# Optimization experiments

Measured on AMD Instinct MI355X. Metric: run time of the kernel, lower is better.

## Reference

```python
import jax, jax.numpy as jnp
import numpy as np

NUM_HEADS = 8
WINDOW = 33  # must be odd for seq length to be preserved


def setup_inputs() -> dict:
    key = jax.random.key(0)
    ks = jax.random.split(key, 7)
    B, S, E = 4, 2048, 256
    sc = 1.0 / np.sqrt(E)
    return {
        "x": jax.random.normal(ks[0], (B, S, E), dtype=jnp.float32),
        "Wq": jax.random.normal(ks[1], (E, E), dtype=jnp.float32) * sc,
        "bq": jax.random.normal(ks[2], (E,), dtype=jnp.float32) * 0.01,
        "Wk": jax.random.normal(ks[3], (E, E), dtype=jnp.float32) * sc,
        "bk": jax.random.normal(ks[4], (E,), dtype=jnp.float32) * 0.01,
        "Wv": jax.random.normal(ks[5], (E, E), dtype=jnp.float32) * sc,
        "bv": jax.random.normal(ks[6], (E,), dtype=jnp.float32) * 0.01,
    }


def reference(x, Wq, bq, Wk, bk, Wv, bv):
    B, S, E = x.shape
    H = NUM_HEADS
    D = E // H
    W = WINDOW
    pad = (W - 1) // 2
    scale = D ** (-0.5)

    def heads(t):  # [B,S,E] -> [B,H,S,D]
        return t.reshape(B, S, H, D).transpose(0, 2, 1, 3)

    q = heads(x @ Wq + bq)
    k = heads(x @ Wk + bk)
    v = heads(x @ Wv + bv)

    K = S - W + 1  # number of k/v windows (unfold with step=1)
    kv_idx = jnp.arange(K)[:, None] + jnp.arange(W)[None, :]  # [K,W]
    k_unf = k[:, :, kv_idx, :]  # [B,H,K,W,D]
    v_unf = v[:, :, kv_idx, :]  # [B,H,K,W,D]

    q_pad = jnp.pad(q, ((0, 0), (0, 0), (pad, pad), (0, 0)))  # zero pad seq
    q_idx = jnp.arange(S)[:, None] + jnp.arange(W)[None, :]  # [S,W]
    q_unf = q_pad[:, :, q_idx, :]  # [B,H,S,W,D]

    # contract over BOTH window and head dim (faithful to the torch einsums)
    scores = jnp.einsum('bhqwd,bhkwd->bhqk', q_unf, k_unf) * scale  # [B,H,S,K]
    attn = jax.nn.softmax(scores, axis=-1)
    out = jnp.einsum('bhqk,bhkwd->bhqd', attn, v_unf)  # sums v over window too
    return out.transpose(0, 2, 1, 3).reshape(B, S, E)
```

## Files before the change

kernel.cpp:

```cpp
#include <hip/hip_runtime.h>
#include <hip/hip_bf16.h>
#include <math.h>

#define BB   4
#define SS   2048
#define EE   256
#define HH   8
#define DD   32
#define WW   33
#define KKN  (SS - WW + 1)
#define SCALE 0.17677669529663687f
#define FMAX 20.0f
#define SCALE2 0.25503486f
#define FM2    28.853900817779268f

typedef __attribute__((ext_vector_type(8))) short short8v;
typedef __attribute__((ext_vector_type(4))) short short4v;
typedef __attribute__((ext_vector_type(4))) float float4v;

__device__ __forceinline__ short f2bf(float f) {
    union { __hip_bfloat16 h; short s; } c;
    c.h = __float2bfloat16(f);
    return c.s;
}

__device__ __forceinline__ float bf2f(short h) {
    union { unsigned u; float f; } c;
    c.u = ((unsigned)(unsigned short)h) << 16;
    return c.f;
}

__device__ __forceinline__ short2 f2bf2(float a, float b) {
    union { __hip_bfloat162 h; short2 s; } c;
    float2 f; f.x = a; f.y = b;
    c.h = __float22bfloat162_rn(f);
    return c.s;
}

#if __has_builtin(__builtin_amdgcn_exp2f)
__device__ __forceinline__ float exp2_fast(float x) { return __builtin_amdgcn_exp2f(x); }
#else
__device__ __forceinline__ float exp2_fast(float x) { return __expf(x * 0.6931471805599453f); }
#endif

__global__ __launch_bounds__(256) void cvt_kernel(
    const float* __restrict__ x,
    const float* __restrict__ Wq, const float* __restrict__ Wk,
    short* __restrict__ xh, short* __restrict__ xl,
    short* __restrict__ wth, short* __restrict__ wtl)
{
    const int t  = threadIdx.x;
    const int bx = blockIdx.x;
    if (bx < 1024) {
        size_t i8 = ((size_t)bx * 256 + t) * 8;
        float4 f0 = *(const float4*)(x + i8);
        float4 f1 = *(const float4*)(x + i8 + 4);
        float f[8] = {f0.x, f0.y, f0.z, f0.w, f1.x, f1.y, f1.z, f1.w};
        short8v h, l;
#pragma unroll
        for (int j = 0; j < 8; j++) {
            short hb = f2bf(f[j]);
            h[j] = hb;
            l[j] = f2bf(f[j] - bf2f(hb));
        }
        *(short8v*)(xh + i8) = h;
        *(short8v*)(xl + i8) = l;
    } else {
        int o   = (bx - 1024) * 2048 + t * 8;
        int mat = o >> 16;
        int rem = o & 65535;
        int n = rem >> 8, k0 = rem & 255;
        const float* W = mat ? Wk : Wq;
        short8v h, l;
#pragma unroll
        for (int j = 0; j < 8; j++) {
            float f = W[(size_t)(k0 + j) * 256 + n];
            short hb = f2bf(f);
            h[j] = hb;
            l[j] = f2bf(f - bf2f(hb));
        }
        *(short8v*)(wth + o) = h;
        *(short8v*)(wtl + o) = l;
    }
}

__global__ __launch_bounds__(256) void qk_mfma_kernel(
    const short* __restrict__ xh, const short* __restrict__ xl,
    const short* __restrict__ wth, const short* __restrict__ wtl,
    const float* __restrict__ bq, const float* __restrict__ bk,
    short* __restrict__ qo, short* __restrict__ ko)
{
    __shared__ alignas(16) short xsh[64][40];
    __shared__ alignas(16) short xsl[64][40];
    __shared__ alignas(16) short wsh[128][40];
    __shared__ alignas(16) short wsl[128][40];

    const int t   = threadIdx.x;
    const int r0  = blockIdx.x * 64;
    const int mat = blockIdx.y >> 1;
    const int cb  = blockIdx.y & 1;
    const int lane = t & 63, wv = t >> 6;
    const int quad = lane >> 4, lr = lane & 15;
    const float* bias = mat ? bk : bq;
    short* op = mat ? ko : qo;
    const size_t wofs = (size_t)(mat * 256 + cb * 128) * 256;
    const short* wthm = wth + wofs;
    const short* wtlm = wtl + wofs;

    float4v acc[8];
#pragma unroll
    for (int ct = 0; ct < 8; ct++) acc[ct] = (float4v){0.f, 0.f, 0.f, 0.f};

    for (int kk = 0; kk < 8; kk++) {
        __syncthreads();
        {
            int r = t >> 2, c8 = (t & 3) * 8;
            size_t go = (size_t)(r0 + r) * 256 + kk * 32 + c8;
            *(short8v*)&xsh[r][c8] = *(const short8v*)(xh + go);
            *(short8v*)&xsl[r][c8] = *(const short8v*)(xl + go);
        }
#pragma unroll
        for (int i = 0; i < 2; i++) {
            int L = t + i * 256;
            int wr = L >> 2, c8 = (L & 3) * 8;
            size_t go = (size_t)wr * 256 + kk * 32 + c8;
            *(short8v*)&wsh[wr][c8] = *(const short8v*)(wthm + go);
            *(short8v*)&wsl[wr][c8] = *(const short8v*)(wtlm + go);
        }
        __syncthreads();

        const short8v ah = *(const short8v*)&xsh[wv * 16 + lr][quad * 8];
        const short8v al = *(const short8v*)&xsl[wv * 16 + lr][quad * 8];
#pragma unroll
        for (int ct = 0; ct < 8; ct++) {
            const short8v bh_ = *(const short8v*)&wsh[ct * 16 + lr][quad * 8];
            const short8v bl_ = *(const short8v*)&wsl[ct * 16 + lr][quad * 8];
            acc[ct] = __builtin_amdgcn_mfma_f32_16x16x32_bf16(ah, bh_, acc[ct], 0, 0, 0);
            acc[ct] = __builtin_amdgcn_mfma_f32_16x16x32_bf16(ah, bl_, acc[ct], 0, 0, 0);
            acc[ct] = __builtin_amdgcn_mfma_f32_16x16x32_bf16(al, bh_, acc[ct], 0, 0, 0);
        }
    }

#pragma unroll
    for (int ct = 0; ct < 8; ct++) {
        int col = cb * 128 + ct * 16 + lr;
        float bv_ = bias[col];
        int h = col >> 5, d = col & 31;
#pragma unroll
        for (int e = 0; e < 4; e++) {
            int row = r0 + wv * 16 + quad * 4 + e;
            int b_ = row >> 11, s = row & 2047;
            size_t o = (((size_t)(b_ * HH + h)) * SS + s) * DD + d;
            op[o] = f2bf(acc[ct][e] + bv_);
        }
    }
}

__global__ __launch_bounds__(256) void qkv_kernel(
    const float* __restrict__ x,
    const float* __restrict__ Wq, const float* __restrict__ bq,
    const float* __restrict__ Wk, const float* __restrict__ bk,
    const float* __restrict__ Wv, const float* __restrict__ bv,
    short* __restrict__ qo, short* __restrict__ ko, float* __restrict__ vo,
    int ct0)
{
    __shared__ alignas(16) float xs[64][68];
    __shared__ alignas(16) float ws[64][68];

    const int t   = threadIdx.x;
    const int r0  = blockIdx.x * 64;
    const int ct  = blockIdx.y + ct0;
    const int mat = ct >> 2;
    const int cm0 = (ct & 3) * 64;
    const float* Wm   = (mat == 0) ? Wq : (mat == 1) ? Wk : Wv;
    const float* bias = (mat == 0) ? bq : (mat == 1) ? bk : bv;

    const int tr = t >> 4, tc = t & 15;

    float acc[4][4];
#pragma unroll
    for (int i = 0; i < 4; i++)
#pragma unroll
        for (int j = 0; j < 4; j++) acc[i][j] = 0.f;

    for (int ec = 0; ec < 4; ec++) {
        const int e0 = ec * 64;
        __syncthreads();
#pragma unroll
        for (int i = 0; i < 4; i++) {
            int L = t + i * 256;
            int r = L >> 4, c4 = (L & 15) * 4;
            *(float4*)&xs[r][c4] = *(const float4*)(x  + (size_t)(r0 + r) * EE + e0 + c4);
            *(float4*)&ws[r][c4] = *(const float4*)(Wm + (size_t)(e0 + r) * EE + cm0 + c4);
        }
        __syncthreads();

#pragma unroll
        for (int eg = 0; eg < 16; eg++) {
            float4 xv[4], wv4[4];
#pragma unroll
            for (int i = 0; i < 4; i++) xv[i]  = *(const float4*)&xs[tr * 4 + i][eg * 4];
#pragma unroll
            for (int j = 0; j < 4; j++) wv4[j] = *(const float4*)&ws[eg * 4 + j][tc * 4];
            const float* w0p = (const float*)&wv4[0];
            const float* w1p = (const float*)&wv4[1];
            const float* w2p = (const float*)&wv4[2];
            const float* w3p = (const float*)&wv4[3];
#pragma unroll
            for (int i = 0; i < 4; i++)
#pragma unroll
                for (int j = 0; j < 4; j++)
                    acc[i][j] = acc[i][j] + xv[i].x * w0p[j] + xv[i].y * w1p[j]
                                          + xv[i].z * w2p[j] + xv[i].w * w3p[j];
        }
    }

    const int cmb = cm0 + tc * 4;
    const int h = cmb >> 5, d0 = cmb & 31;
    float b4[4];
#pragma unroll
    for (int j = 0; j < 4; j++) b4[j] = bias[cmb + j];

#pragma unroll
    for (int i = 0; i < 4; i++) {
        int row = r0 + tr * 4 + i;
        int b_  = row >> 11;
        int s   = row & 2047;
        size_t o = (((size_t)(b_ * HH + h)) * SS + s) * DD + d0;
        if (mat == 2) {
            float4 vv;
            vv.x = acc[i][0] + b4[0]; vv.y = acc[i][1] + b4[1];
            vv.z = acc[i][2] + b4[2]; vv.w = acc[i][3] + b4[3];
            *(float4*)(vo + o) = vv;
        } else {
            short4v sv;
            sv.x = f2bf(acc[i][0] + b4[0]); sv.y = f2bf(acc[i][1] + b4[1]);
            sv.z = f2bf(acc[i][2] + b4[2]); sv.w = f2bf(acc[i][3] + b4[3]);
            *(short4v*)(((mat == 0) ? qo : ko) + o) = sv;
        }
    }
}

__global__ __launch_bounds__(64) void vs_kernel(
    const float* __restrict__ v, short* __restrict__ vsT)
{
    const int t   = threadIdx.x;
    const int d4  = t & 7;
    const int kkb = blockIdx.x * 8 + (t >> 3);
    const int bh  = blockIdx.y;
    if (kkb >= 252) return;
    const int kb0 = kkb * 8;

    const float4* vp = (const float4*)(v + ((size_t)bh * SS + kb0) * DD) + d4;
    float4 rbuf[7];
    float4 acc = {0.f, 0.f, 0.f, 0.f};
#pragma unroll
    for (int w = 0; w < WW; w++) {
        float4 xv = vp[w * 8];
        if (w < 7) rbuf[w] = xv;
        acc.x += xv.x; acc.y += xv.y; acc.z += xv.z; acc.w += xv.w;
    }
    short8v sh[4];
    sh[0][0] = f2bf(acc.x); sh[1][0] = f2bf(acc.y);
    sh[2][0] = f2bf(acc.z); sh[3][0] = f2bf(acc.w);
#pragma unroll
    for (int s = 1; s < 8; s++) {
        float4 sub = rbuf[s - 1];
        float4 add = vp[(s + 32) * 8];
        acc.x += add.x - sub.x; acc.y += add.y - sub.y;
        acc.z += add.z - sub.z; acc.w += add.w - sub.w;
        sh[0][s] = f2bf(acc.x); sh[1][s] = f2bf(acc.y);
        sh[2][s] = f2bf(acc.z); sh[3][s] = f2bf(acc.w);
    }
#pragma unroll
    for (int j = 0; j < 4; j++) {
        short* op = vsT + ((size_t)bh * DD + 4 * d4 + j) * KKN + kb0;
        *(short8v*)op = sh[j];
    }
}

__global__ __launch_bounds__(256, 4) void attn_kernel(
    const short* __restrict__ qg, const short* __restrict__ kg,
    const short* __restrict__ vsTg, float* __restrict__ out)
{
    __shared__ alignas(16) short QbS[64][40];
    __shared__ alignas(16) short Kb[96][40];
    __shared__ alignas(16) short Gst[96][72];
    __shared__ alignas(16) short vT[32][72];
    __shared__ float lrow[32];

    short (*Qb)[40] = QbS;
    short (*pb)[72] = (short (*)[72])QbS;

    const int t  = threadIdx.x;
    const int qt = blockIdx.x;
    const int bh = blockIdx.y;
    const int q0 = qt * 32;

    const short* qb   = qg   + (size_t)bh * SS * DD;
    const short* kb   = kg   + (size_t)bh * SS * DD;
    const short* vsTb = vsTg + (size_t)bh * DD * KKN;

    const int lane = t & 63, wv = t >> 6;
    const int quad = lane >> 4, lr = lane & 15;
    const int ptm = wv >> 1, ptn = wv & 1;
    const int jcol = 64 + (t & 7);

    const int qitw  = wv & 1;
    const int tbase = wv >> 1;
    const int qi    = qitw * 16 + lr;

    const int vd  = t >> 3, vc8 = (t & 7) * 8;
    const int r2  = t >> 2, c8r = (t & 3) * 8;

    {
        short8v z = {0, 0, 0, 0, 0, 0, 0, 0};
        short* g = &Gst[0][0];
        for (int i = t; i < 864; i += 256) *(short8v*)(g + 8 * i) = z;
    }

    {
        int gq = q0 - 16 + r2;
        if (gq >= 0 && gq < SS) {
            *(short8v*)&Qb[r2][c8r] = *(const short8v*)(qb + (size_t)gq * DD + c8r);
        } else {
            float4 z = {0.f, 0.f, 0.f, 0.f};
            *(float4*)&Qb[r2][c8r] = z;
        }
        *(short8v*)&Kb[r2][c8r] = *(const short8v*)(kb + (size_t)r2 * DD + c8r);
        if (t < 128)
            *(short8v*)&Kb[64 + r2][c8r] = *(const short8v*)(kb + (size_t)(64 + r2) * DD + c8r);
    }
    if (t < 32) lrow[t] = 0.f;
    __syncthreads();

    short8v Qf[4];
#pragma unroll
    for (int tq = 0; tq < 4; tq++)
        Qf[tq] = *(const short8v*)&Qb[tq * 16 + lr][quad * 8];

    short8v Ufw[2];
#pragma unroll
    for (int ch = 0; ch < 2; ch++) {
        short8v u;
#pragma unroll
        for (int j = 0; j < 8; j++) {
            int m = ch * 32 + quad * 8 + j;
            u[j] = (qi <= m && m <= qi + 32) ? (short)0x3F80 : (short)0;
        }
        Ufw[ch] = u;
    }

    float4v acc = {0.f, 0.f, 0.f, 0.f};
    float lsumw = 0.f;
    const int npass = (wv < 2) ? 2 : 1;
    int k0m = 0;

    for (int kt = 0; kt < 32; kt++) {
        const int k0 = kt * 64;
        for (int pass = 0; pass < npass; pass++) {
            const int tk = wv + pass * 4;
            int krow = k0m + tk * 16 + lr; if (krow >= 96) krow -= 96;
            const short8v A = *(const short8v*)&Kb[krow][quad * 8];
#pragma unroll
            for (int tq = 0; tq < 4; tq++) {
                const int del = tk - tq;
                if (del < -2 || del > 4) continue;
                float4v c0 = {0.f, 0.f, 0.f, 0.f};
                c0 = __builtin_amdgcn_mfma_f32_16x16x32_bf16(A, Qf[tq], c0, 0, 0, 0);
                const int i   = tq * 16 + lr;
                const int j2b = tk * 16 + quad * 4 - i + 31;
                short* gbase = &Gst[0][i];
                short2 g01 = f2bf2(c0[0], c0[1]);
                short2 g23 = f2bf2(c0[2], c0[3]);
                short gv[4] = {g01.x, g01.y, g23.x, g23.y};
#pragma unroll
                for (int e = 0; e < 4; e++) {
                    int j2 = j2b + e;
                    short* dst = ((unsigned)j2 < 95u) ? (gbase + j2 * 72)
                                                      : (gbase + 95 * 72);
                    *dst = gv[e];
                }
            }
        }

        if (kt > 0) {
            const short8v Ap0 = *(const short8v*)&pb[ptm * 16 + lr][quad * 8];
            const short8v Ap1 = *(const short8v*)&pb[ptm * 16 + lr][32 + quad * 8];
            const short8v Bv0 = *(const short8v*)&vT[ptn * 16 + lr][quad * 8];
            const short8v Bv1 = *(const short8v*)&vT[ptn * 16 + lr][32 + quad * 8];
            __builtin_amdgcn_s_setprio(1);
            acc = __builtin_amdgcn_mfma_f32_16x16x32_bf16(Ap0, Bv0, acc, 0, 0, 0);
            acc = __builtin_amdgcn_mfma_f32_16x16x32_bf16(Ap1, Bv1, acc, 0, 0, 0);
            __builtin_amdgcn_s_setprio(0);
        }
        __syncthreads();

        {
            int col = k0 + vc8; if (col > KKN - 8) col = KKN - 8;
            *(short8v*)&vT[vd][vc8] = *(const short8v*)(vsTb + (size_t)vd * KKN + col);
        }
        if (kt < 31) {
            int gp = k0 + 96 + r2;
            int ga = (gp < SS) ? gp : (SS - 1);
            int slot = k0m + r2; if (slot >= 96) slot -= 96;
            *(short8v*)&Kb[slot][c8r] = *(const short8v*)(kb + (size_t)ga * DD + c8r);
        }

        const unsigned lim = (kt == 31) ? 32u : 64u;
        if (kt == 31) {
            short4v z4 = {0, 0, 0, 0};
            int zr = t >> 3, zc = (t & 7) * 4 + 32;
            *(short4v*)&pb[zr][zc] = z4;
        }

        short* prow = &pb[qi][0];
#pragma unroll
        for (int u = 0; u < 3; u++) {
            const int tile = 2 * u + tbase;
            const int jrow = tile * 16 + lr;
            const short8v A0f = *(const short8v*)&Gst[jrow][quad * 8];
            const short8v A1f = *(const short8v*)&Gst[jrow][32 + quad * 8];
            float4v D = {0.f, 0.f, 0.f, 0.f};
            __builtin_amdgcn_s_setprio(1);
            D = __builtin_amdgcn_mfma_f32_16x16x32_bf16(A0f, Ufw[0], D, 0, 0, 0);
            D = __builtin_amdgcn_mfma_f32_16x16x32_bf16(A1f, Ufw[1], D, 0, 0, 0);
            __builtin_amdgcn_s_setprio(0);
            const int kib = qi + tile * 16 + quad * 4 - 31;
            float p0 = exp2_fast(fmaf(D[0], SCALE2, -FM2));
            float p1 = exp2_fast(fmaf(D[1], SCALE2, -FM2));
            float p2 = exp2_fast(fmaf(D[2], SCALE2, -FM2));
            float p3 = exp2_fast(fmaf(D[3], SCALE2, -FM2));
            short2 c01 = f2bf2(p0, p1);
            short2 c23 = f2bf2(p2, p3);
            float pv[4] = {p0, p1, p2, p3};
            short cv[4] = {c01.x, c01.y, c23.x, c23.y};
#pragma unroll
            for (int e = 0; e < 4; e++) {
                int ki = kib + e;
                bool ok = (unsigned)ki < lim;
                short* dst = ok ? (prow + ki) : (prow + jcol);
                *dst = cv[e];
                lsumw += ok ? pv[e] : 0.f;
            }
        }
        __syncthreads();
        k0m += 64; if (k0m >= 96) k0m -= 96;
    }

    {
        const short8v Ap0 = *(const short8v*)&pb[ptm * 16 + lr][quad * 8];
        const short8v Ap1 = *(const short8v*)&pb[ptm * 16 + lr][32 + quad * 8];
        const short8v Bv0 = *(const short8v*)&vT[ptn * 16 + lr][quad * 8];
        const short8v Bv1 = *(const short8v*)&vT[ptn * 16 + lr][32 + quad * 8];
        acc = __builtin_amdgcn_mfma_f32_16x16x32_bf16(Ap0, Bv0, acc, 0, 0, 0);
        acc = __builtin_amdgcn_mfma_f32_16x16x32_bf16(Ap1, Bv1, acc, 0, 0, 0);
    }

    {
        float s = lsumw;
        s += __shfl_xor(s, 16);
        s += __shfl_xor(s, 32);
        if (quad == 0) atomicAdd(&lrow[qitw * 16 + lr], s);
    }
    __syncthreads();

    {
        const int rrow = ptm * 16 + quad * 4;
        const int col  = ptn * 16 + lr;
        const int b_ = bh >> 3, h = bh & 7;
#pragma unroll
        for (int e = 0; e < 4; e++) {
            int s_ = q0 + rrow + e;
            out[((size_t)(b_ * SS + s_)) * EE + h * DD + col] = acc[e] / lrow[rrow + e];
        }
    }
}

extern "C" void kernel_launch(void* const* d_in, const int* in_sizes, int n_in,
                              void* d_out, int out_size, void* d_ws, size_t ws_size,
                              hipStream_t stream)
{
    (void)in_sizes; (void)n_in; (void)out_size; (void)ws_size;
    const float* x  = (const float*)d_in[0];
    const float* Wq = (const float*)d_in[1];
    const float* bq = (const float*)d_in[2];
    const float* Wk = (const float*)d_in[3];
    const float* bk = (const float*)d_in[4];
    const float* Wv = (const float*)d_in[5];
    const float* bv = (const float*)d_in[6];
    float* out = (float*)d_out;

    const size_t REG = (size_t)BB * HH * SS * DD;
    short* qbf   = (short*)d_ws;
    short* kbf   = qbf + REG;
    float* vbuf  = (float*)(kbf + REG);
    short* vsTb  = (short*)(vbuf + REG);

    short* xh  = (short*)vbuf;
    short* xl  = xh + REG;
    short* wth = (short*)out;
    short* wtl = wth + 2 * 256 * 256;

    cvt_kernel<<<dim3(1088), dim3(256), 0, stream>>>(x, Wq, Wk, xh, xl, wth, wtl);
    qk_mfma_kernel<<<dim3(128, 4), dim3(256), 0, stream>>>(xh, xl, wth, wtl,
                                                           bq, bk, qbf, kbf);
    qkv_kernel<<<dim3(128, 4), dim3(256), 0, stream>>>(x, Wq, bq, Wk, bk, Wv, bv,
                                                       qbf, kbf, vbuf, 8);
    vs_kernel<<<dim3(32, 32), dim3(64), 0, stream>>>(vbuf, vsTb);
    attn_kernel<<<dim3(64, 32), dim3(256), 0, stream>>>(qbf, kbf, vsTb, out);
}
```

Measured before the change: 262.7 us.

## Fuse x bf16 split into projection and move V projection onto MFMA path

The x hi/lo bf16 split now happens inside the projection kernel while it loads tiles, so the separate pass that wrote xh/xl to global memory is gone. The FP32 scalar V projection kernel is dropped, and V is computed by the same split-bf16 MFMA kernel with the grid extended to six column blocks. This cuts one launch, a full round trip of x through global memory, and the slow FP32 FMA GEMM for V. In exchange each block redoes the x conversion, and V now goes through a three-term bf16 approximation instead of exact FP32.

```diff
diff --git a/kernel.cpp b/kernel.cpp
--- a/kernel.cpp
+++ b/kernel.cpp
@@ -44,51 +44,35 @@
 #endif
 
 __global__ __launch_bounds__(256) void cvt_kernel(
-    const float* __restrict__ x,
     const float* __restrict__ Wq, const float* __restrict__ Wk,
-    short* __restrict__ xh, short* __restrict__ xl,
+    const float* __restrict__ Wv,
     short* __restrict__ wth, short* __restrict__ wtl)
 {
     const int t  = threadIdx.x;
     const int bx = blockIdx.x;
-    if (bx < 1024) {
-        size_t i8 = ((size_t)bx * 256 + t) * 8;
-        float4 f0 = *(const float4*)(x + i8);
-        float4 f1 = *(const float4*)(x + i8 + 4);
-        float f[8] = {f0.x, f0.y, f0.z, f0.w, f1.x, f1.y, f1.z, f1.w};
-        short8v h, l;
-#pragma unroll
-        for (int j = 0; j < 8; j++) {
-            short hb = f2bf(f[j]);
-            h[j] = hb;
-            l[j] = f2bf(f[j] - bf2f(hb));
-        }
-        *(short8v*)(xh + i8) = h;
-        *(short8v*)(xl + i8) = l;
-    } else {
-        int o   = (bx - 1024) * 2048 + t * 8;
-        int mat = o >> 16;
-        int rem = o & 65535;
-        int n = rem >> 8, k0 = rem & 255;
-        const float* W = mat ? Wk : Wq;
-        short8v h, l;
-#pragma unroll
-        for (int j = 0; j < 8; j++) {
-            float f = W[(size_t)(k0 + j) * 256 + n];
-            short hb = f2bf(f);
-            h[j] = hb;
-            l[j] = f2bf(f - bf2f(hb));
-        }
-        *(short8v*)(wth + o) = h;
-        *(short8v*)(wtl + o) = l;
-    }
-}
-
-__global__ __launch_bounds__(256) void qk_mfma_kernel(
-    const short* __restrict__ xh, const short* __restrict__ xl,
+    int o   = bx * 2048 + t * 8;
+    int mat = o >> 16;
+    int rem = o & 65535;
+    int n = rem >> 8, k0 = rem & 255;
+    const float* W = (mat == 0) ? Wq : (mat == 1) ? Wk : Wv;
+    short8v h, l;
+#pragma unroll
+    for (int j = 0; j < 8; j++) {
+        float f = W[(size_t)(k0 + j) * 256 + n];
+        short hb = f2bf(f);
+        h[j] = hb;
+        l[j] = f2bf(f - bf2f(hb));
+    }
+    *(short8v*)(wth + o) = h;
+    *(short8v*)(wtl + o) = l;
+}
+
+__global__ __launch_bounds__(256) void proj_kernel(
+    const float* __restrict__ x,
     const short* __restrict__ wth, const short* __restrict__ wtl,
     const float* __restrict__ bq, const float* __restrict__ bk,
-    short* __restrict__ qo, short* __restrict__ ko)
+    const float* __restrict__ bv,
+    short* __restrict__ qo, short* __restrict__ ko, float* __restrict__ vo)
 {
     __shared__ alignas(16) short xsh[64][40];
     __shared__ alignas(16) short xsl[64][40];
@@ -101,8 +85,7 @@
     const int cb  = blockIdx.y & 1;
     const int lane = t & 63, wv = t >> 6;
     const int quad = lane >> 4, lr = lane & 15;
-    const float* bias = mat ? bk : bq;
-    short* op = mat ? ko : qo;
+    const float* bias = (mat == 0) ? bq : (mat == 1) ? bk : bv;
     const size_t wofs = (size_t)(mat * 256 + cb * 128) * 256;
     const short* wthm = wth + wofs;
     const short* wtlm = wtl + wofs;
@@ -115,9 +98,19 @@
         __syncthreads();
         {
             int r = t >> 2, c8 = (t & 3) * 8;
-            size_t go = (size_t)(r0 + r) * 256 + kk * 32 + c8;
-            *(short8v*)&xsh[r][c8] = *(const short8v*)(xh + go);
-            *(short8v*)&xsl[r][c8] = *(const short8v*)(xl + go);
+            const float* xp = x + (size_t)(r0 + r) * 256 + kk * 32 + c8;
+            float4 f0 = *(const float4*)xp;
+            float4 f1 = *(const float4*)(xp + 4);
+            float f[8] = {f0.x, f0.y, f0.z, f0.w, f1.x, f1.y, f1.z, f1.w};
+            short8v h, l;
+#pragma unroll
+            for (int j = 0; j < 8; j++) {
+                short hb = f2bf(f[j]);
+                h[j] = hb;
+                l[j] = f2bf(f[j] - bf2f(hb));
+            }
+            *(short8v*)&xsh[r][c8] = h;
+            *(short8v*)&xsl[r][c8] = l;
         }
 #pragma unroll
         for (int i = 0; i < 2; i++) {
@@ -141,6 +134,7 @@
         }
     }
 
+    short* op = (mat == 0) ? qo : ko;
 #pragma unroll
     for (int ct = 0; ct < 8; ct++) {
         int col = cb * 128 + ct * 16 + lr;
@@ -151,92 +145,8 @@
             int row = r0 + wv * 16 + quad * 4 + e;
             int b_ = row >> 11, s = row & 2047;
             size_t o = (((size_t)(b_ * HH + h)) * SS + s) * DD + d;
-            op[o] = f2bf(acc[ct][e] + bv_);
-        }
-    }
-}
-
-__global__ __launch_bounds__(256) void qkv_kernel(
-    const float* __restrict__ x,
-    const float* __restrict__ Wq, const float* __restrict__ bq,
-    const float* __restrict__ Wk, const float* __restrict__ bk,
-    const float* __restrict__ Wv, const float* __restrict__ bv,
-    short* __restrict__ qo, short* __restrict__ ko, float* __restrict__ vo,
-    int ct0)
-{
-    __shared__ alignas(16) float xs[64][68];
-    __shared__ alignas(16) float ws[64][68];
-
-    const int t   = threadIdx.x;
-    const int r0  = blockIdx.x * 64;
-    const int ct  = blockIdx.y + ct0;
-    const int mat = ct >> 2;
-    const int cm0 = (ct & 3) * 64;
-    const float* Wm   = (mat == 0) ? Wq : (mat == 1) ? Wk : Wv;
-    const float* bias = (mat == 0) ? bq : (mat == 1) ? bk : bv;
-
-    const int tr = t >> 4, tc = t & 15;
-
-    float acc[4][4];
-#pragma unroll
-    for (int i = 0; i < 4; i++)
-#pragma unroll
-        for (int j = 0; j < 4; j++) acc[i][j] = 0.f;
-
-    for (int ec = 0; ec < 4; ec++) {
-        const int e0 = ec * 64;
-        __syncthreads();
-#pragma unroll
-        for (int i = 0; i < 4; i++) {
-            int L = t + i * 256;
-            int r = L >> 4, c4 = (L & 15) * 4;
-            *(float4*)&xs[r][c4] = *(const float4*)(x  + (size_t)(r0 + r) * EE + e0 + c4);
-            *(float4*)&ws[r][c4] = *(const float4*)(Wm + (size_t)(e0 + r) * EE + cm0 + c4);
-        }
-        __syncthreads();
-
-#pragma unroll
-        for (int eg = 0; eg < 16; eg++) {
-            float4 xv[4], wv4[4];
-#pragma unroll
-            for (int i = 0; i < 4; i++) xv[i]  = *(const float4*)&xs[tr * 4 + i][eg * 4];
-#pragma unroll
-            for (int j = 0; j < 4; j++) wv4[j] = *(const float4*)&ws[eg * 4 + j][tc * 4];
-            const float* w0p = (const float*)&wv4[0];
-            const float* w1p = (const float*)&wv4[1];
-            const float* w2p = (const float*)&wv4[2];
-            const float* w3p = (const float*)&wv4[3];
-#pragma unroll
-            for (int i = 0; i < 4; i++)
-#pragma unroll
-                for (int j = 0; j < 4; j++)
-                    acc[i][j] = acc[i][j] + xv[i].x * w0p[j] + xv[i].y * w1p[j]
-                                          + xv[i].z * w2p[j] + xv[i].w * w3p[j];
-        }
-    }
-
-    const int cmb = cm0 + tc * 4;
-    const int h = cmb >> 5, d0 = cmb & 31;
-    float b4[4];
-#pragma unroll
-    for (int j = 0; j < 4; j++) b4[j] = bias[cmb + j];
-
-#pragma unroll
-    for (int i = 0; i < 4; i++) {
-        int row = r0 + tr * 4 + i;
-        int b_  = row >> 11;
-        int s   = row & 2047;
-        size_t o = (((size_t)(b_ * HH + h)) * SS + s) * DD + d0;
-        if (mat == 2) {
-            float4 vv;
-            vv.x = acc[i][0] + b4[0]; vv.y = acc[i][1] + b4[1];
-            vv.z = acc[i][2] + b4[2]; vv.w = acc[i][3] + b4[3];
-            *(float4*)(vo + o) = vv;
-        } else {
-            short4v sv;
-            sv.x = f2bf(acc[i][0] + b4[0]); sv.y = f2bf(acc[i][1] + b4[1]);
-            sv.z = f2bf(acc[i][2] + b4[2]); sv.w = f2bf(acc[i][3] + b4[3]);
-            *(short4v*)(((mat == 0) ? qo : ko) + o) = sv;
+            if (mat == 2) vo[o] = acc[ct][e] + bv_;
+            else          op[o] = f2bf(acc[ct][e] + bv_);
         }
     }
 }
@@ -497,16 +407,13 @@
     float* vbuf  = (float*)(kbf + REG);
     short* vsTb  = (short*)(vbuf + REG);
 
-    short* xh  = (short*)vbuf;
-    short* xl  = xh + REG;
     short* wth = (short*)out;
-    short* wtl = wth + 2 * 256 * 256;
-
-    cvt_kernel<<<dim3(1088), dim3(256), 0, stream>>>(x, Wq, Wk, xh, xl, wth, wtl);
-    qk_mfma_kernel<<<dim3(128, 4), dim3(256), 0, stream>>>(xh, xl, wth, wtl,
-                                                           bq, bk, qbf, kbf);
-    qkv_kernel<<<dim3(128, 4), dim3(256), 0, stream>>>(x, Wq, bq, Wk, bk, Wv, bv,
-                                                       qbf, kbf, vbuf, 8);
+    short* wtl = wth + 3 * 256 * 256;
+
+    cvt_kernel<<<dim3(96), dim3(256), 0, stream>>>(Wq, Wk, Wv, wth, wtl);
+    proj_kernel<<<dim3(128, 6), dim3(256), 0, stream>>>(x, wth, wtl,
+                                                        bq, bk, bv,
+                                                        qbf, kbf, vbuf);
     vs_kernel<<<dim3(32, 32), dim3(64), 0, stream>>>(vbuf, vsTb);
     attn_kernel<<<dim3(64, 32), dim3(256), 0, stream>>>(qbf, kbf, vsTb, out);
 }
```

Measured after the change: 249.7 us. 1.05x faster.
